# Kernel tuning notes

Measured on AMD Instinct MI355X. Metric: run time of the kernel, lower is better.

## Reference

```python
import jax, jax.numpy as jnp
import numpy as np

B, N, C = 4, 2048, 1024
H = 8
D = C // H  # head dim = 128
SCALE = D ** -0.5
EPS = 1e-5


def setup_inputs() -> dict:
    key = jax.random.key(0)
    ks = jax.random.split(key, 12)
    s = 0.02
    return {
        "x": jax.random.normal(ks[0], (B, N, C), jnp.float32),
        "ln1_g": jnp.ones((C,), jnp.float32),
        "ln1_b": jnp.zeros((C,), jnp.float32),
        "w_qkv": jax.random.normal(ks[1], (3 * C, C), jnp.float32) * s,  # torch Linear weight [out,in], no bias
        "w_proj": jax.random.normal(ks[2], (C, C), jnp.float32) * s,
        "b_proj": jnp.zeros((C,), jnp.float32),
        "ln2_g": jnp.ones((C,), jnp.float32),
        "ln2_b": jnp.zeros((C,), jnp.float32),
        "w1": jax.random.normal(ks[3], (C, C), jnp.float32) * s,
        "b1": jnp.full((C,), 0.1, jnp.float32),
        "w2": jax.random.normal(ks[4], (C, C), jnp.float32) * s,
        "b2": jnp.full((C,), 0.1, jnp.float32),
        "bn_g": jnp.ones((C,), jnp.float32),
        "bn_b": jnp.zeros((C,), jnp.float32),
        "bn_mean": jnp.zeros((C,), jnp.float32),
        "bn_var": jnp.ones((C,), jnp.float32),
    }


def _layernorm(x, g, b):
    mu = jnp.mean(x, axis=-1, keepdims=True)
    var = jnp.mean(jnp.square(x - mu), axis=-1, keepdims=True)
    return (x - mu) * jax.lax.rsqrt(var + EPS) * g + b


def reference(x, ln1_g, ln1_b, w_qkv, w_proj, b_proj, ln2_g, ln2_b,
              w1, b1, w2, b2, bn_g, bn_b, bn_mean, bn_var):
    # --- attention branch (pre-LN) ---
    h = _layernorm(x, ln1_g, ln1_b)
    qkv = h @ w_qkv.T                              # [B,N,3C]
    qkv = qkv.reshape(B, N, 3, H, D)
    q = qkv[:, :, 0].transpose(0, 2, 1, 3)         # [B,H,N,D]
    k = qkv[:, :, 1].transpose(0, 2, 1, 3)
    v = qkv[:, :, 2].transpose(0, 2, 1, 3)
    attn = jnp.einsum('bhnd,bhmd->bhnm', q, k) * SCALE
    attn = jax.nn.softmax(attn, axis=-1)
    o = jnp.einsum('bhnm,bhmd->bhnd', attn, v)     # [B,H,N,D]
    o = o.transpose(0, 2, 1, 3).reshape(B, N, C)
    x = x + (o @ w_proj.T + b_proj)

    # --- MLP branch (pre-LN), ELU + eval-mode BatchNorm ---
    h = _layernorm(x, ln2_g, ln2_b)
    h = jax.nn.elu(h @ w1.T + b1)
    h = jax.nn.elu(h @ w2.T + b2)
    h = (h - bn_mean) * jax.lax.rsqrt(bn_var + EPS) * bn_g + bn_b
    return x + h
```

## Files before the change

kernel.cpp:

```cpp
#include <hip/hip_runtime.h>
#include <hip/hip_bf16.h>

using u16 = unsigned short;
typedef __attribute__((ext_vector_type(8))) __bf16 bf16x8;
typedef __attribute__((ext_vector_type(4))) float f32x4;
typedef __attribute__((ext_vector_type(16))) float f32x16;
typedef __attribute__((ext_vector_type(4))) unsigned int u32x4;
typedef __attribute__((ext_vector_type(2))) unsigned int u32x2;

#define LN_EPS 1e-5f
#define ATT_SCALE 0.08838834764831845f

__device__ __forceinline__ u16 f2bf(float f) {
    unsigned int u = __builtin_bit_cast(unsigned int, f);
    u += 0x7FFFu + ((u >> 16) & 1u);
    return (u16)(u >> 16);
}

__device__ __forceinline__ bf16x8 ld_frag(const u16* p) {
    return __builtin_bit_cast(bf16x8, *(const u32x4*)p);
}

__device__ __forceinline__ unsigned pack_bf2(float lo, float hi) {
    return __builtin_amdgcn_perm(__builtin_bit_cast(unsigned, hi),
                                 __builtin_bit_cast(unsigned, lo), 0x07060302u);
}

__device__ __forceinline__ void gl_lds(const u16* g, u16* l) {
    __builtin_amdgcn_global_load_lds((const __attribute__((address_space(1))) void*)g,
                                     (__attribute__((address_space(3))) void*)l, 16, 0, 0);
}

__global__ __launch_bounds__(256)
void cvt_ln(const float* __restrict__ x, const float* __restrict__ g,
            const float* __restrict__ b, u16* __restrict__ hout,
            const float* __restrict__ w_qkv, const float* __restrict__ w_proj,
            const float* __restrict__ w1, const float* __restrict__ w2,
            u16* __restrict__ wout)
{
    const int t = threadIdx.x;
    if (blockIdx.x < 8192) {
        const int row = blockIdx.x;
        const float4 v = ((const float4*)(x + (size_t)row * 1024))[t];
        float s  = v.x + v.y + v.z + v.w;
        float ss = v.x * v.x + v.y * v.y + v.z * v.z + v.w * v.w;
        #pragma unroll
        for (int d = 32; d > 0; d >>= 1) { s += __shfl_down(s, d); ss += __shfl_down(ss, d); }
        __shared__ float red[8];
        const int wave = t >> 6, lane = t & 63;
        if (lane == 0) { red[wave] = s; red[4 + wave] = ss; }
        __syncthreads();
        const float S  = red[0] + red[1] + red[2] + red[3];
        const float SS = red[4] + red[5] + red[6] + red[7];
        const float mu = S * (1.f / 1024.f);
        const float rstd = rsqrtf(SS * (1.f / 1024.f) - mu * mu + LN_EPS);
        const float4 gv = ((const float4*)g)[t];
        const float4 bv = ((const float4*)b)[t];
        ushort4 ov;
        ov.x = f2bf((v.x - mu) * rstd * gv.x + bv.x);
        ov.y = f2bf((v.y - mu) * rstd * gv.y + bv.y);
        ov.z = f2bf((v.z - mu) * rstd * gv.z + bv.z);
        ov.w = f2bf((v.w - mu) * rstd * gv.w + bv.w);
        ((ushort4*)(hout + (size_t)row * 1024))[t] = ov;
    } else {
        const int i = (blockIdx.x - 8192) * 256 + t;
        const int n_qkv = 3072 * 1024 / 4, n_c = 1024 * 1024 / 4;
        const float* src;
        int j = i;
        if (j < n_qkv) { src = w_qkv; }
        else if ((j -= n_qkv) < n_c) { src = w_proj; }
        else if ((j -= n_c) < n_c)   { src = w1; }
        else { j -= n_c; src = w2; }
        const float4 v = ((const float4*)src)[j];
        ushort4 o;
        o.x = f2bf(v.x); o.y = f2bf(v.y); o.z = f2bf(v.z); o.w = f2bf(v.w);
        ((ushort4*)wout)[i] = o;
    }
}

__global__ __launch_bounds__(256)
void ln_kernel(const float* __restrict__ x, const float* __restrict__ g,
               const float* __restrict__ b, u16* __restrict__ out)
{
    const int row = blockIdx.x;
    const int t = threadIdx.x;
    const float4 v = ((const float4*)(x + (size_t)row * 1024))[t];
    float s  = v.x + v.y + v.z + v.w;
    float ss = v.x * v.x + v.y * v.y + v.z * v.z + v.w * v.w;
    #pragma unroll
    for (int d = 32; d > 0; d >>= 1) { s += __shfl_down(s, d); ss += __shfl_down(ss, d); }
    __shared__ float red[8];
    const int wave = t >> 6, lane = t & 63;
    if (lane == 0) { red[wave] = s; red[4 + wave] = ss; }
    __syncthreads();
    const float S  = red[0] + red[1] + red[2] + red[3];
    const float SS = red[4] + red[5] + red[6] + red[7];
    const float mu = S * (1.f / 1024.f);
    const float rstd = rsqrtf(SS * (1.f / 1024.f) - mu * mu + LN_EPS);
    const float4 gv = ((const float4*)g)[t];
    const float4 bv = ((const float4*)b)[t];
    ushort4 ov;
    ov.x = f2bf((v.x - mu) * rstd * gv.x + bv.x);
    ov.y = f2bf((v.y - mu) * rstd * gv.y + bv.y);
    ov.z = f2bf((v.z - mu) * rstd * gv.z + bv.z);
    ov.w = f2bf((v.w - mu) * rstd * gv.w + bv.w);
    ((ushort4*)(out + (size_t)row * 1024))[t] = ov;
}


#define GEMM_PREAMBLE(Aptr, Bptr, Kdim)                                           \
    __shared__ __align__(16) u16 As[128 * 64];                                    \
    __shared__ __align__(16) u16 Bs[128 * 64];                                    \
    const int tid  = threadIdx.x;                                                 \
    const int wave = tid >> 6;                                                    \
    const int lane = tid & 63;                                                    \
    const int quad = lane >> 4;                                                   \
    const int l16  = lane & 15;                                                   \
    const int m0 = blockIdx.x * 128;                                              \
    const int n0 = blockIdx.y * 128;                                              \
    const int wm = (wave & 1) * 64;                                               \
    const int wn = (wave >> 1) * 64;                                              \
    f32x4 acc[4][4];                                                              \
    _Pragma("unroll")                                                             \
    for (int i = 0; i < 4; i++)                                                   \
        _Pragma("unroll")                                                         \
        for (int j = 0; j < 4; j++)                                               \
            acc[i][j] = f32x4{0.f, 0.f, 0.f, 0.f};                                \
    const int srow8 = lane >> 3;                  \
    const int scol  = ((lane & 7) ^ srow8) * 8;    \
    const u16* gA = Aptr + (size_t)(m0 + wave * 8 + srow8) * Kdim + scol;         \
    const u16* gB = Bptr + (size_t)(n0 + wave * 8 + srow8) * Kdim + scol;         \
    u16* lA = &As[wave * 512];                                                    \
    u16* lB = &Bs[wave * 512];                                                    \
    for (int k0 = 0; k0 < Kdim; k0 += 64) {                                       \
        _Pragma("unroll")                                                         \
        for (int rnd = 0; rnd < 4; rnd++) {                                       \
            gl_lds(gA + (size_t)rnd * 32 * Kdim + k0, lA + rnd * 2048);           \
            gl_lds(gB + (size_t)rnd * 32 * Kdim + k0, lB + rnd * 2048);           \
        }                                                                         \
        __syncthreads();                                                          \
        _Pragma("unroll")                                                         \
        for (int kk = 0; kk < 2; kk++) {                                          \
            bf16x8 af[4], bfv[4];                                                 \
            _Pragma("unroll")                                                     \
            for (int i = 0; i < 4; i++) {                                         \
                const int row = wm + i * 16 + l16;                                \
                const int c = (kk * 4 + quad) ^ (row & 7);                        \
                af[i] = ld_frag(&As[row * 64 + c * 8]);                           \
            }                                                                     \
            _Pragma("unroll")                                                     \
            for (int j = 0; j < 4; j++) {                                         \
                const int row = wn + j * 16 + l16;                                \
                const int c = (kk * 4 + quad) ^ (row & 7);                        \
                bfv[j] = ld_frag(&Bs[row * 64 + c * 8]);                          \
            }                                                                     \
            _Pragma("unroll")                                                     \
            for (int i = 0; i < 4; i++)                                           \
                _Pragma("unroll")                                                 \
                for (int j = 0; j < 4; j++)                                       \
                    acc[i][j] = __builtin_amdgcn_mfma_f32_16x16x32_bf16(          \
                        af[i], bfv[j], acc[i][j], 0, 0, 0);                       \
        }                                                                         \
        __syncthreads();                                                          \
    }

__global__ __launch_bounds__(256, 3)
void gemm_qkv(const u16* __restrict__ A, const u16* __restrict__ Bw,
              u16* __restrict__ Cb, u16* __restrict__ Cv)
{
    GEMM_PREAMBLE(A, Bw, 1024)

    #pragma unroll
    for (int j = 0; j < 4; j++) {
        const int gn = n0 + wn + j * 16 + l16;
        if (gn < 2048) {
            const float qs = (gn < 1024) ? ATT_SCALE : 1.0f;
            #pragma unroll
            for (int i = 0; i < 4; i++) {
                const int gm0 = m0 + wm + i * 16 + quad * 4;
                #pragma unroll
                for (int r = 0; r < 4; r++)
                    Cb[(size_t)(gm0 + r) * 2048 + gn] = f2bf(acc[i][j][r] * qs);
            }
        } else {
            const int hh = (gn >> 7) & 7, dd = gn & 127;
            #pragma unroll
            for (int i = 0; i < 4; i++) {
                const int gm0 = m0 + wm + i * 16 + quad * 4;
                #pragma unroll
                for (int r = 0; r < 4; r++) {
                    const int tok = gm0 + r;
                    Cv[((size_t)((tok >> 11) * 8 + hh) * 128 + dd) * 2048 + (tok & 2047)] =
                        f2bf(acc[i][j][r]);
                }
            }
        }
    }
}

template <int EPI>
__global__ __launch_bounds__(256, 3)
void gemm_c(const u16* __restrict__ A, const u16* __restrict__ Bw,
            const float* __restrict__ bias, const float* __restrict__ res,
            float* __restrict__ Cf, u16* __restrict__ Cb,
            const float* __restrict__ bng, const float* __restrict__ bnb,
            const float* __restrict__ bnm, const float* __restrict__ bnv)
{
    const int N = 1024;
    GEMM_PREAMBLE(A, Bw, 1024)

    #pragma unroll
    for (int j = 0; j < 4; j++) {
        const int gn = n0 + wn + j * 16 + l16;
        float bs = bias[gn], sc = 0.f, sh = 0.f;
        if constexpr (EPI == 3) {
            const float iv = rsqrtf(bnv[gn] + LN_EPS);
            sc = bng[gn] * iv;
            sh = bnb[gn] - bnm[gn] * sc;
        }
        #pragma unroll
        for (int i = 0; i < 4; i++) {
            const int gm0 = m0 + wm + i * 16 + quad * 4;
            #pragma unroll
            for (int r = 0; r < 4; r++) {
                const size_t idx = (size_t)(gm0 + r) * N + gn;
                const float v = acc[i][j][r];
                if constexpr (EPI == 1) {
                    Cf[idx] = res[idx] + v + bs;
                } else if constexpr (EPI == 2) {
                    float t = v + bs;
                    t = t > 0.f ? t : (__expf(t) - 1.f);
                    Cb[idx] = f2bf(t);
                } else {
                    float t = v + bs;
                    t = t > 0.f ? t : (__expf(t) - 1.f);
                    t = t * sc + sh;
                    Cf[idx] = res[idx] + t;
                }
            }
        }
    }
}

__global__ __launch_bounds__(256, 2)
void attn_kernel(const u16* __restrict__ qk, const u16* __restrict__ vT, u16* __restrict__ o)
{
    __shared__ __align__(16) u16 smem[32768];

    const int tid  = threadIdx.x;
    const int wave = tid >> 6;
    const int lane = tid & 63;
    const int l32  = lane & 31;
    const int hl   = lane >> 5;
    const int id   = blockIdx.x;
    const int bh   = ((id >> 7) << 3) | (id & 7);
    const int qt   = (id >> 3) & 15;
    const int b    = bh >> 3, h = bh & 7;
    const size_t tok0 = (size_t)b * 2048;

    const u16* qptr = qk + h * 128;
    const u16* kptr = qk + 1024 + h * 128;
    const u16* vptr = vT + (size_t)bh * 128 * 2048;

    #pragma unroll
    for (int qq = 0; qq < 8; qq++) {
        const int s = qq * 256 + tid;
        const int r = s >> 4;
        const int cg = (s & 15) ^ (r & 7);
        const u16* g = qptr + (tok0 + qt * 128 + r) * 2048 + cg * 8;
        const int sb = 16384 + (qq * 256 + (tid & 192)) * 8;
        gl_lds(g, smem + sb);
    }
    __syncthreads();

    bf16x8 qf[8];
    {
        const int row = wave * 32 + l32;
        #pragma unroll
        for (int ks = 0; ks < 8; ks++) {
            const int c = (ks * 2 + hl) ^ (row & 7);
            qf[ks] = ld_frag(smem + 16384 + row * 128 + c * 8);
        }
    }

    f32x16 oacc[4];
    #pragma unroll
    for (int i = 0; i < 4; i++)
        #pragma unroll
        for (int e = 0; e < 16; e++) oacc[i][e] = 0.f;
    float l_acc = 0.f;

    {
        #pragma unroll
        for (int qq = 0; qq < 4; qq++) {
            const int s = qq * 256 + tid;
            const int rk = s >> 4, ck = (s & 15) ^ (rk & 7);
            gl_lds(kptr + (tok0 + rk) * 2048 + ck * 8,
                   smem + (qq * 256 + (tid & 192)) * 8);
            const int rv = s >> 3, cv = (s & 7) ^ (rv & 7);
            gl_lds(vptr + (size_t)rv * 2048 + cv * 8,
                   smem + 8192 + (qq * 256 + (tid & 192)) * 8);
        }
    }

    for (int kt = 0; kt < 32; kt++) {
        __syncthreads();

        if (kt + 1 < 32) {
            u16* nb = smem + ((kt + 1) & 1) * 16384;
            #pragma unroll
            for (int qq = 0; qq < 4; qq++) {
                const int s = qq * 256 + tid;
                const int rk = s >> 4, ck = (s & 15) ^ (rk & 7);
                gl_lds(kptr + (tok0 + (kt + 1) * 64 + rk) * 2048 + ck * 8,
                       nb + (qq * 256 + (tid & 192)) * 8);
                const int rv = s >> 3, cv = (s & 7) ^ (rv & 7);
                gl_lds(vptr + (size_t)rv * 2048 + (kt + 1) * 64 + cv * 8,
                       nb + 8192 + (qq * 256 + (tid & 192)) * 8);
            }
        }

        const u16* Ks = smem + (kt & 1) * 16384;
        const u16* Vs = Ks + 8192;

        f32x16 sacc[2];
        #pragma unroll
        for (int t = 0; t < 2; t++)
            #pragma unroll
            for (int e = 0; e < 16; e++) sacc[t][e] = 0.f;
        __builtin_amdgcn_s_setprio(1);
        #pragma unroll
        for (int ks = 0; ks < 8; ks++) {
            #pragma unroll
            for (int mt = 0; mt < 2; mt++) {
                const int row = mt * 32 + l32;
                const int c = (ks * 2 + hl) ^ (row & 7);
                const bf16x8 kf = ld_frag(Ks + row * 128 + c * 8);
                sacc[mt] = __builtin_amdgcn_mfma_f32_32x32x16_bf16(kf, qf[ks], sacc[mt], 0, 0, 0);
            }
        }
        __builtin_amdgcn_s_setprio(0);

        unsigned pk[2][8];
        #pragma unroll
        for (int t = 0; t < 2; t++) {
            #pragma unroll
            for (int r2 = 0; r2 < 8; r2++) {
                const float p0 = __expf(sacc[t][2 * r2]);
                const float p1 = __expf(sacc[t][2 * r2 + 1]);
                l_acc += p0 + p1;
                pk[t][r2] = pack_bf2(p0, p1);
            }
        }

        #pragma unroll
        for (int ks = 0; ks < 4; ks++) {
            const int t = ks >> 1;
            const int pb = (ks & 1) * 4;
            const u32x2 r02 = __builtin_amdgcn_permlane32_swap(pk[t][pb + 0], pk[t][pb + 2], false, false);
            const u32x2 r13 = __builtin_amdgcn_permlane32_swap(pk[t][pb + 1], pk[t][pb + 3], false, false);
            u32x4 pu;
            pu.x = r02.x; pu.y = r13.x; pu.z = r02.y; pu.w = r13.y;
            const bf16x8 pf = __builtin_bit_cast(bf16x8, pu);
            __builtin_amdgcn_s_setprio(1);
            #pragma unroll
            for (int dt = 0; dt < 4; dt++) {
                const int row = dt * 32 + l32;
                const int c = (ks * 2 + hl) ^ (row & 7);
                const bf16x8 vf = ld_frag(Vs + row * 64 + c * 8);
                oacc[dt] = __builtin_amdgcn_mfma_f32_32x32x16_bf16(vf, pf, oacc[dt], 0, 0, 0);
            }
            __builtin_amdgcn_s_setprio(0);
        }
    }

    __syncthreads();
    u16* Ot = smem;
    const float lt  = l_acc + __shfl_xor(l_acc, 32);
    const float inv = 1.0f / lt;
    const int qloc = wave * 32 + l32;
    #pragma unroll
    for (int dt = 0; dt < 4; dt++) {
        #pragma unroll
        for (int r2 = 0; r2 < 8; r2++) {
            const float v0 = oacc[dt][2 * r2] * inv;
            const float v1 = oacc[dt][2 * r2 + 1] * inv;
            const int dp = dt * 32 + 4 * hl + 2 * (r2 & 1) + 8 * (r2 >> 1);
            *(unsigned*)(Ot + qloc * 136 + dp) = pack_bf2(v0, v1);
        }
    }
    __syncthreads();
    const int qr = tid >> 1;
    const int hh = tid & 1;
    const u16* src = Ot + qr * 136 + hh * 64;
    u16* dst = o + (tok0 + qt * 128 + qr) * 1024 + h * 128 + hh * 64;
    #pragma unroll
    for (int c = 0; c < 8; c++)
        *(u32x4*)(dst + c * 8) = *(const u32x4*)(src + c * 8);
}

extern "C" void kernel_launch(void* const* d_in, const int* in_sizes, int n_in,
                              void* d_out, int out_size, void* d_ws, size_t ws_size,
                              hipStream_t stream)
{
    const float* x      = (const float*)d_in[0];
    const float* ln1_g  = (const float*)d_in[1];
    const float* ln1_b  = (const float*)d_in[2];
    const float* w_qkv  = (const float*)d_in[3];
    const float* w_proj = (const float*)d_in[4];
    const float* b_proj = (const float*)d_in[5];
    const float* ln2_g  = (const float*)d_in[6];
    const float* ln2_b  = (const float*)d_in[7];
    const float* w1     = (const float*)d_in[8];
    const float* b1     = (const float*)d_in[9];
    const float* w2     = (const float*)d_in[10];
    const float* b2     = (const float*)d_in[11];
    const float* bn_g   = (const float*)d_in[12];
    const float* bn_b   = (const float*)d_in[13];
    const float* bn_m   = (const float*)d_in[14];
    const float* bn_v   = (const float*)d_in[15];
    float* out = (float*)d_out;

    u16* wq   = (u16*)d_ws;
    u16* wp   = wq  + (size_t)3072 * 1024;
    u16* w1b  = wp  + (size_t)1024 * 1024;
    u16* w2b  = w1b + (size_t)1024 * 1024;
    u16* hbuf = w2b + (size_t)1024 * 1024;
    u16* qkb  = hbuf + (size_t)8192 * 1024;
    u16* vTb  = qkb + (size_t)8192 * 2048;
    u16* obuf = vTb + (size_t)8192 * 1024;
    float* x1 = (float*)(obuf + (size_t)8192 * 1024);

    cvt_ln<<<14336, 256, 0, stream>>>(x, ln1_g, ln1_b, hbuf, w_qkv, w_proj, w1, w2, wq);

    gemm_qkv<<<dim3(64, 24), 256, 0, stream>>>(hbuf, wq, qkb, vTb);

    attn_kernel<<<512, 256, 0, stream>>>(qkb, vTb, obuf);

    gemm_c<1><<<dim3(64, 8), 256, 0, stream>>>(obuf, wp,
        b_proj, x, x1, nullptr, nullptr, nullptr, nullptr, nullptr);

    ln_kernel<<<8192, 256, 0, stream>>>(x1, ln2_g, ln2_b, hbuf);

    gemm_c<2><<<dim3(64, 8), 256, 0, stream>>>(hbuf, w1b,
        b1, nullptr, nullptr, obuf, nullptr, nullptr, nullptr, nullptr);

    gemm_c<3><<<dim3(64, 8), 256, 0, stream>>>(obuf, w2b,
        b2, x1, out, nullptr, bn_g, bn_b, bn_m, bn_v);
}
```

Before: 361.8 us.

## Process two query sub-tiles per wave in attention to reuse K/V fragments

The attention kernel now handles 256 queries per block, 64 per wave, as two 32-row sub-tiles, instead of 128. Each K and V fragment loaded from LDS feeds two MFMAs, which halves LDS traffic and the K/V global loads per query. The grid shrinks to 256 blocks with launch bounds relaxed to one block per SM, and the output writeback is split into two phases through shared memory. In exchange, register pressure roughly doubles for the accumulators, occupancy drops, and 256 blocks may not fill all compute units well.

```diff
diff --git a/kernel.cpp b/kernel.cpp
--- a/kernel.cpp
+++ b/kernel.cpp
@@ -107,7 +107,6 @@
     ((ushort4*)(out + (size_t)row * 1024))[t] = ov;
 }
 
-
 #define GEMM_PREAMBLE(Aptr, Bptr, Kdim)                                           \
     __shared__ __align__(16) u16 As[128 * 64];                                    \
     __shared__ __align__(16) u16 Bs[128 * 64];                                    \
@@ -126,8 +125,8 @@
         _Pragma("unroll")                                                         \
         for (int j = 0; j < 4; j++)                                               \
             acc[i][j] = f32x4{0.f, 0.f, 0.f, 0.f};                                \
-    const int srow8 = lane >> 3;                  \
-    const int scol  = ((lane & 7) ^ srow8) * 8;    \
+    const int srow8 = lane >> 3;                                                  \
+    const int scol  = ((lane & 7) ^ srow8) * 8;                                   \
     const u16* gA = Aptr + (size_t)(m0 + wave * 8 + srow8) * Kdim + scol;         \
     const u16* gB = Bptr + (size_t)(n0 + wave * 8 + srow8) * Kdim + scol;         \
     u16* lA = &As[wave * 512];                                                    \
@@ -242,7 +241,7 @@
     }
 }
 
-__global__ __launch_bounds__(256, 2)
+__global__ __launch_bounds__(256, 1)
 void attn_kernel(const u16* __restrict__ qk, const u16* __restrict__ vT, u16* __restrict__ o)
 {
     __shared__ __align__(16) u16 smem[32768];
@@ -253,8 +252,8 @@
     const int l32  = lane & 31;
     const int hl   = lane >> 5;
     const int id   = blockIdx.x;
-    const int bh   = ((id >> 7) << 3) | (id & 7);
-    const int qt   = (id >> 3) & 15;
+    const int bh   = id & 31;
+    const int qt   = id >> 5;
     const int b    = bh >> 3, h = bh & 7;
     const size_t tok0 = (size_t)b * 2048;
 
@@ -263,32 +262,35 @@
     const u16* vptr = vT + (size_t)bh * 128 * 2048;
 
     #pragma unroll
-    for (int qq = 0; qq < 8; qq++) {
+    for (int qq = 0; qq < 16; qq++) {
         const int s = qq * 256 + tid;
         const int r = s >> 4;
         const int cg = (s & 15) ^ (r & 7);
-        const u16* g = qptr + (tok0 + qt * 128 + r) * 2048 + cg * 8;
-        const int sb = 16384 + (qq * 256 + (tid & 192)) * 8;
-        gl_lds(g, smem + sb);
+        gl_lds(qptr + (tok0 + qt * 256 + r) * 2048 + cg * 8,
+               smem + (qq * 256 + (tid & 192)) * 8);
     }
     __syncthreads();
 
-    bf16x8 qf[8];
-    {
-        const int row = wave * 32 + l32;
+    bf16x8 qf[2][8];
+    #pragma unroll
+    for (int qh = 0; qh < 2; qh++) {
+        const int row = wave * 64 + qh * 32 + l32;
         #pragma unroll
         for (int ks = 0; ks < 8; ks++) {
             const int c = (ks * 2 + hl) ^ (row & 7);
-            qf[ks] = ld_frag(smem + 16384 + row * 128 + c * 8);
-        }
-    }
-
-    f32x16 oacc[4];
+            qf[qh][ks] = ld_frag(smem + row * 128 + c * 8);
+        }
+    }
+    __syncthreads();
+
+    f32x16 oacc[4][2];
     #pragma unroll
     for (int i = 0; i < 4; i++)
         #pragma unroll
-        for (int e = 0; e < 16; e++) oacc[i][e] = 0.f;
-    float l_acc = 0.f;
+        for (int qh = 0; qh < 2; qh++)
+            #pragma unroll
+            for (int e = 0; e < 16; e++) oacc[i][qh][e] = 0.f;
+    float l_acc[2] = {0.f, 0.f};
 
     {
         #pragma unroll
@@ -323,11 +325,13 @@
         const u16* Ks = smem + (kt & 1) * 16384;
         const u16* Vs = Ks + 8192;
 
-        f32x16 sacc[2];
+        f32x16 sacc[2][2];
         #pragma unroll
         for (int t = 0; t < 2; t++)
             #pragma unroll
-            for (int e = 0; e < 16; e++) sacc[t][e] = 0.f;
+            for (int qh = 0; qh < 2; qh++)
+                #pragma unroll
+                for (int e = 0; e < 16; e++) sacc[t][qh][e] = 0.f;
         __builtin_amdgcn_s_setprio(1);
         #pragma unroll
         for (int ks = 0; ks < 8; ks++) {
@@ -336,20 +340,26 @@
                 const int row = mt * 32 + l32;
                 const int c = (ks * 2 + hl) ^ (row & 7);
                 const bf16x8 kf = ld_frag(Ks + row * 128 + c * 8);
-                sacc[mt] = __builtin_amdgcn_mfma_f32_32x32x16_bf16(kf, qf[ks], sacc[mt], 0, 0, 0);
+                #pragma unroll
+                for (int qh = 0; qh < 2; qh++)
+                    sacc[mt][qh] = __builtin_amdgcn_mfma_f32_32x32x16_bf16(
+                        kf, qf[qh][ks], sacc[mt][qh], 0, 0, 0);
             }
         }
         __builtin_amdgcn_s_setprio(0);
 
-        unsigned pk[2][8];
+        unsigned pk[2][2][8];
         #pragma unroll
         for (int t = 0; t < 2; t++) {
             #pragma unroll
-            for (int r2 = 0; r2 < 8; r2++) {
-                const float p0 = __expf(sacc[t][2 * r2]);
-                const float p1 = __expf(sacc[t][2 * r2 + 1]);
-                l_acc += p0 + p1;
-                pk[t][r2] = pack_bf2(p0, p1);
+            for (int qh = 0; qh < 2; qh++) {
+                #pragma unroll
+                for (int r2 = 0; r2 < 8; r2++) {
+                    const float p0 = __expf(sacc[t][qh][2 * r2]);
+                    const float p1 = __expf(sacc[t][qh][2 * r2 + 1]);
+                    l_acc[qh] += p0 + p1;
+                    pk[t][qh][r2] = pack_bf2(p0, p1);
+                }
             }
         }
 
@@ -357,46 +367,64 @@
         for (int ks = 0; ks < 4; ks++) {
             const int t = ks >> 1;
             const int pb = (ks & 1) * 4;
-            const u32x2 r02 = __builtin_amdgcn_permlane32_swap(pk[t][pb + 0], pk[t][pb + 2], false, false);
-            const u32x2 r13 = __builtin_amdgcn_permlane32_swap(pk[t][pb + 1], pk[t][pb + 3], false, false);
-            u32x4 pu;
-            pu.x = r02.x; pu.y = r13.x; pu.z = r02.y; pu.w = r13.y;
-            const bf16x8 pf = __builtin_bit_cast(bf16x8, pu);
-            __builtin_amdgcn_s_setprio(1);
+            bf16x8 vf[4];
             #pragma unroll
             for (int dt = 0; dt < 4; dt++) {
                 const int row = dt * 32 + l32;
                 const int c = (ks * 2 + hl) ^ (row & 7);
-                const bf16x8 vf = ld_frag(Vs + row * 64 + c * 8);
-                oacc[dt] = __builtin_amdgcn_mfma_f32_32x32x16_bf16(vf, pf, oacc[dt], 0, 0, 0);
-            }
-            __builtin_amdgcn_s_setprio(0);
-        }
-    }
-
-    __syncthreads();
-    u16* Ot = smem;
-    const float lt  = l_acc + __shfl_xor(l_acc, 32);
-    const float inv = 1.0f / lt;
-    const int qloc = wave * 32 + l32;
-    #pragma unroll
-    for (int dt = 0; dt < 4; dt++) {
-        #pragma unroll
-        for (int r2 = 0; r2 < 8; r2++) {
-            const float v0 = oacc[dt][2 * r2] * inv;
-            const float v1 = oacc[dt][2 * r2 + 1] * inv;
-            const int dp = dt * 32 + 4 * hl + 2 * (r2 & 1) + 8 * (r2 >> 1);
-            *(unsigned*)(Ot + qloc * 136 + dp) = pack_bf2(v0, v1);
-        }
-    }
-    __syncthreads();
-    const int qr = tid >> 1;
-    const int hh = tid & 1;
-    const u16* src = Ot + qr * 136 + hh * 64;
-    u16* dst = o + (tok0 + qt * 128 + qr) * 1024 + h * 128 + hh * 64;
-    #pragma unroll
-    for (int c = 0; c < 8; c++)
-        *(u32x4*)(dst + c * 8) = *(const u32x4*)(src + c * 8);
+                vf[dt] = ld_frag(Vs + row * 64 + c * 8);
+            }
+            #pragma unroll
+            for (int qh = 0; qh < 2; qh++) {
+                const u32x2 r02 = __builtin_amdgcn_permlane32_swap(pk[t][qh][pb + 0], pk[t][qh][pb + 2], false, false);
+                const u32x2 r13 = __builtin_amdgcn_permlane32_swap(pk[t][qh][pb + 1], pk[t][qh][pb + 3], false, false);
+                u32x4 pu;
+                pu.x = r02.x; pu.y = r13.x; pu.z = r02.y; pu.w = r13.y;
+                const bf16x8 pf = __builtin_bit_cast(bf16x8, pu);
+                __builtin_amdgcn_s_setprio(1);
+                #pragma unroll
+                for (int dt = 0; dt < 4; dt++)
+                    oacc[dt][qh] = __builtin_amdgcn_mfma_f32_32x32x16_bf16(
+                        vf[dt], pf, oacc[dt][qh], 0, 0, 0);
+                __builtin_amdgcn_s_setprio(0);
+            }
+        }
+    }
+
+    const float lt0 = l_acc[0] + __shfl_xor(l_acc[0], 32);
+    const float lt1 = l_acc[1] + __shfl_xor(l_acc[1], 32);
+    const float inv0 = 1.0f / lt0;
+    const float inv1 = 1.0f / lt1;
+
+    #pragma unroll
+    for (int ph = 0; ph < 2; ph++) {
+        __syncthreads();
+        if ((wave >> 1) == ph) {
+            #pragma unroll
+            for (int qh = 0; qh < 2; qh++) {
+                const float inv = (qh == 0) ? inv0 : inv1;
+                const int qloc = (wave & 1) * 64 + qh * 32 + l32;
+                #pragma unroll
+                for (int dt = 0; dt < 4; dt++) {
+                    #pragma unroll
+                    for (int r2 = 0; r2 < 8; r2++) {
+                        const float v0 = oacc[dt][qh][2 * r2] * inv;
+                        const float v1 = oacc[dt][qh][2 * r2 + 1] * inv;
+                        const int dp = dt * 32 + 4 * hl + 2 * (r2 & 1) + 8 * (r2 >> 1);
+                        *(unsigned*)(smem + qloc * 136 + dp) = pack_bf2(v0, v1);
+                    }
+                }
+            }
+        }
+        __syncthreads();
+        const int qr = tid >> 1;
+        const int hh = tid & 1;
+        const u16* src = smem + qr * 136 + hh * 64;
+        u16* dst = o + (tok0 + qt * 256 + ph * 128 + qr) * 1024 + h * 128 + hh * 64;
+        #pragma unroll
+        for (int c = 0; c < 8; c++)
+            *(u32x4*)(dst + c * 8) = *(const u32x4*)(src + c * 8);
+    }
 }
 
 extern "C" void kernel_launch(void* const* d_in, const int* in_sizes, int n_in,
@@ -435,7 +463,7 @@
 
     gemm_qkv<<<dim3(64, 24), 256, 0, stream>>>(hbuf, wq, qkb, vTb);
 
-    attn_kernel<<<512, 256, 0, stream>>>(qkb, vTb, obuf);
+    attn_kernel<<<256, 256, 0, stream>>>(qkb, vTb, obuf);
 
     gemm_c<1><<<dim3(64, 8), 256, 0, stream>>>(obuf, wp,
         b_proj, x, x1, nullptr, nullptr, nullptr, nullptr, nullptr);
```

After: 392.1 us. 1.08x slower.

## Split attention KV tile across wave pairs, each wave owning 64 query rows

Applied to the files above, without the earlier changes.

Each wave now handles 64 query rows (two 32-row subtiles) but only half of each 64-key tile. Every K and V fragment loaded from LDS therefore feeds two MFMAs, which halves LDS reads per MFMA. The two key-halves' partial outputs and row sums are merged through shared memory at the end. The cost is double the accumulator registers (128 fp32 for oacc), which puts the 2-blocks-per-CU occupancy at risk, plus an extra reduction stage with two more barriers.

```diff
diff --git a/kernel.cpp b/kernel.cpp
--- a/kernel.cpp
+++ b/kernel.cpp
@@ -107,7 +107,6 @@
     ((ushort4*)(out + (size_t)row * 1024))[t] = ov;
 }
 
-
 #define GEMM_PREAMBLE(Aptr, Bptr, Kdim)                                           \
     __shared__ __align__(16) u16 As[128 * 64];                                    \
     __shared__ __align__(16) u16 Bs[128 * 64];                                    \
@@ -126,8 +125,8 @@
         _Pragma("unroll")                                                         \
         for (int j = 0; j < 4; j++)                                               \
             acc[i][j] = f32x4{0.f, 0.f, 0.f, 0.f};                                \
-    const int srow8 = lane >> 3;                  \
-    const int scol  = ((lane & 7) ^ srow8) * 8;    \
+    const int srow8 = lane >> 3;                                                  \
+    const int scol  = ((lane & 7) ^ srow8) * 8;                                   \
     const u16* gA = Aptr + (size_t)(m0 + wave * 8 + srow8) * Kdim + scol;         \
     const u16* gB = Bptr + (size_t)(n0 + wave * 8 + srow8) * Kdim + scol;         \
     u16* lA = &As[wave * 512];                                                    \
@@ -245,13 +244,15 @@
 __global__ __launch_bounds__(256, 2)
 void attn_kernel(const u16* __restrict__ qk, const u16* __restrict__ vT, u16* __restrict__ o)
 {
-    __shared__ __align__(16) u16 smem[32768];
+    __shared__ __align__(16) u16 smem[33024];
 
     const int tid  = threadIdx.x;
     const int wave = tid >> 6;
     const int lane = tid & 63;
     const int l32  = lane & 31;
     const int hl   = lane >> 5;
+    const int qh2  = wave & 1;
+    const int kh   = wave >> 1;
     const int id   = blockIdx.x;
     const int bh   = ((id >> 7) << 3) | (id & 7);
     const int qt   = (id >> 3) & 15;
@@ -273,22 +274,25 @@
     }
     __syncthreads();
 
-    bf16x8 qf[8];
-    {
-        const int row = wave * 32 + l32;
+    bf16x8 qf[2][8];
+    #pragma unroll
+    for (int qs = 0; qs < 2; qs++) {
+        const int row = qh2 * 64 + qs * 32 + l32;
         #pragma unroll
         for (int ks = 0; ks < 8; ks++) {
             const int c = (ks * 2 + hl) ^ (row & 7);
-            qf[ks] = ld_frag(smem + 16384 + row * 128 + c * 8);
-        }
-    }
-
-    f32x16 oacc[4];
+            qf[qs][ks] = ld_frag(smem + 16384 + row * 128 + c * 8);
+        }
+    }
+
+    f32x16 oacc[4][2];
     #pragma unroll
     for (int i = 0; i < 4; i++)
         #pragma unroll
-        for (int e = 0; e < 16; e++) oacc[i][e] = 0.f;
-    float l_acc = 0.f;
+        for (int qs = 0; qs < 2; qs++)
+            #pragma unroll
+            for (int e = 0; e < 16; e++) oacc[i][qs][e] = 0.f;
+    float l_acc[2] = {0.f, 0.f};
 
     {
         #pragma unroll
@@ -325,68 +329,125 @@
 
         f32x16 sacc[2];
         #pragma unroll
-        for (int t = 0; t < 2; t++)
-            #pragma unroll
-            for (int e = 0; e < 16; e++) sacc[t][e] = 0.f;
+        for (int qs = 0; qs < 2; qs++)
+            #pragma unroll
+            for (int e = 0; e < 16; e++) sacc[qs][e] = 0.f;
         __builtin_amdgcn_s_setprio(1);
         #pragma unroll
         for (int ks = 0; ks < 8; ks++) {
-            #pragma unroll
-            for (int mt = 0; mt < 2; mt++) {
-                const int row = mt * 32 + l32;
-                const int c = (ks * 2 + hl) ^ (row & 7);
-                const bf16x8 kf = ld_frag(Ks + row * 128 + c * 8);
-                sacc[mt] = __builtin_amdgcn_mfma_f32_32x32x16_bf16(kf, qf[ks], sacc[mt], 0, 0, 0);
-            }
+            const int row = kh * 32 + l32;
+            const int c = (ks * 2 + hl) ^ (row & 7);
+            const bf16x8 kf = ld_frag(Ks + row * 128 + c * 8);
+            #pragma unroll
+            for (int qs = 0; qs < 2; qs++)
+                sacc[qs] = __builtin_amdgcn_mfma_f32_32x32x16_bf16(kf, qf[qs][ks], sacc[qs], 0, 0, 0);
         }
         __builtin_amdgcn_s_setprio(0);
 
         unsigned pk[2][8];
         #pragma unroll
-        for (int t = 0; t < 2; t++) {
+        for (int qs = 0; qs < 2; qs++) {
             #pragma unroll
             for (int r2 = 0; r2 < 8; r2++) {
-                const float p0 = __expf(sacc[t][2 * r2]);
-                const float p1 = __expf(sacc[t][2 * r2 + 1]);
-                l_acc += p0 + p1;
-                pk[t][r2] = pack_bf2(p0, p1);
-            }
-        }
-
-        #pragma unroll
-        for (int ks = 0; ks < 4; ks++) {
-            const int t = ks >> 1;
-            const int pb = (ks & 1) * 4;
-            const u32x2 r02 = __builtin_amdgcn_permlane32_swap(pk[t][pb + 0], pk[t][pb + 2], false, false);
-            const u32x2 r13 = __builtin_amdgcn_permlane32_swap(pk[t][pb + 1], pk[t][pb + 3], false, false);
-            u32x4 pu;
-            pu.x = r02.x; pu.y = r13.x; pu.z = r02.y; pu.w = r13.y;
-            const bf16x8 pf = __builtin_bit_cast(bf16x8, pu);
-            __builtin_amdgcn_s_setprio(1);
+                const float p0 = __expf(sacc[qs][2 * r2]);
+                const float p1 = __expf(sacc[qs][2 * r2 + 1]);
+                l_acc[qs] += p0 + p1;
+                pk[qs][r2] = pack_bf2(p0, p1);
+            }
+        }
+
+        #pragma unroll
+        for (int ks2 = 0; ks2 < 2; ks2++) {
+            bf16x8 vf[4];
             #pragma unroll
             for (int dt = 0; dt < 4; dt++) {
                 const int row = dt * 32 + l32;
-                const int c = (ks * 2 + hl) ^ (row & 7);
-                const bf16x8 vf = ld_frag(Vs + row * 64 + c * 8);
-                oacc[dt] = __builtin_amdgcn_mfma_f32_32x32x16_bf16(vf, pf, oacc[dt], 0, 0, 0);
-            }
-            __builtin_amdgcn_s_setprio(0);
+                const int c = (kh * 4 + ks2 * 2 + hl) ^ (row & 7);
+                vf[dt] = ld_frag(Vs + row * 64 + c * 8);
+            }
+            #pragma unroll
+            for (int qs = 0; qs < 2; qs++) {
+                const int pb = ks2 * 4;
+                const u32x2 r02 = __builtin_amdgcn_permlane32_swap(pk[qs][pb + 0], pk[qs][pb + 2], false, false);
+                const u32x2 r13 = __builtin_amdgcn_permlane32_swap(pk[qs][pb + 1], pk[qs][pb + 3], false, false);
+                u32x4 pu;
+                pu.x = r02.x; pu.y = r13.x; pu.z = r02.y; pu.w = r13.y;
+                const bf16x8 pf = __builtin_bit_cast(bf16x8, pu);
+                __builtin_amdgcn_s_setprio(1);
+                #pragma unroll
+                for (int dt = 0; dt < 4; dt++)
+                    oacc[dt][qs] = __builtin_amdgcn_mfma_f32_32x32x16_bf16(vf[dt], pf, oacc[dt][qs], 0, 0, 0);
+                __builtin_amdgcn_s_setprio(0);
+            }
         }
     }
 
     __syncthreads();
+    float lt[2];
+    lt[0] = l_acc[0] + __shfl_xor(l_acc[0], 32);
+    lt[1] = l_acc[1] + __shfl_xor(l_acc[1], 32);
+
+    float* const ox = (float*)smem;
+    float* const lx = (float*)(smem + 32768);
+
+    if (kh == 1) {
+        #pragma unroll
+        for (int qs = 0; qs < 2; qs++) {
+            #pragma unroll
+            for (int dt = 0; dt < 4; dt++) {
+                const int base16 = qh2 * 2048 + qs * 1024 + dt * 256;
+                #pragma unroll
+                for (int c = 0; c < 4; c++) {
+                    const int cc = c ^ (lane & 3);
+                    const int ch = base16 + lane * 4 + cc;
+                    *(f32x4*)(ox + ch * 4) = f32x4{oacc[dt][qs][cc * 4 + 0],
+                                                   oacc[dt][qs][cc * 4 + 1],
+                                                   oacc[dt][qs][cc * 4 + 2],
+                                                   oacc[dt][qs][cc * 4 + 3]};
+                }
+            }
+            if (hl == 0) lx[qh2 * 64 + qs * 32 + l32] = lt[qs];
+        }
+    }
+    __syncthreads();
+    if (kh == 0) {
+        #pragma unroll
+        for (int qs = 0; qs < 2; qs++) {
+            #pragma unroll
+            for (int dt = 0; dt < 4; dt++) {
+                const int base16 = qh2 * 2048 + qs * 1024 + dt * 256;
+                #pragma unroll
+                for (int c = 0; c < 4; c++) {
+                    const int cc = c ^ (lane & 3);
+                    const int ch = base16 + lane * 4 + cc;
+                    const f32x4 v = *(const f32x4*)(ox + ch * 4);
+                    oacc[dt][qs][cc * 4 + 0] += v[0];
+                    oacc[dt][qs][cc * 4 + 1] += v[1];
+                    oacc[dt][qs][cc * 4 + 2] += v[2];
+                    oacc[dt][qs][cc * 4 + 3] += v[3];
+                }
+            }
+            lt[qs] += lx[qh2 * 64 + qs * 32 + l32];
+        }
+    }
+    __syncthreads();
+
     u16* Ot = smem;
-    const float lt  = l_acc + __shfl_xor(l_acc, 32);
-    const float inv = 1.0f / lt;
-    const int qloc = wave * 32 + l32;
-    #pragma unroll
-    for (int dt = 0; dt < 4; dt++) {
-        #pragma unroll
-        for (int r2 = 0; r2 < 8; r2++) {
-            const float v0 = oacc[dt][2 * r2] * inv;
-            const float v1 = oacc[dt][2 * r2 + 1] * inv;
-            const int dp = dt * 32 + 4 * hl + 2 * (r2 & 1) + 8 * (r2 >> 1);
-            *(unsigned*)(Ot + qloc * 136 + dp) = pack_bf2(v0, v1);
+    if (kh == 0) {
+        #pragma unroll
+        for (int qs = 0; qs < 2; qs++) {
+            const float inv = 1.0f / lt[qs];
+            const int qloc = qh2 * 64 + qs * 32 + l32;
+            #pragma unroll
+            for (int dt = 0; dt < 4; dt++) {
+                #pragma unroll
+                for (int r2 = 0; r2 < 8; r2++) {
+                    const float v0 = oacc[dt][qs][2 * r2] * inv;
+                    const float v1 = oacc[dt][qs][2 * r2 + 1] * inv;
+                    const int dp = dt * 32 + 4 * hl + 2 * (r2 & 1) + 8 * (r2 >> 1);
+                    *(unsigned*)(Ot + qloc * 136 + dp) = pack_bf2(v0, v1);
+                }
+            }
         }
     }
     __syncthreads();
```

New measurement: 529.0 us. 46.2% more time.

## Double-buffer GEMM LDS tiles to overlap global loads with MFMA

Applied to the files above, without the earlier changes.

Converts the shared GEMM main loop to a two-stage LDS ping-pong. The next K tile is prefetched with direct global-to-LDS loads while MFMAs run on the current tile, and one barrier per iteration replaces two. It also raises wave priority around the MFMA block and lowers the launch-bounds occupancy hint from 3 to 2 to account for the doubled LDS use. The cost is lower occupancy and a possible hazard, since gl_lds writes must be complete before the next barrier's reads.

```diff
diff --git a/kernel.cpp b/kernel.cpp
--- a/kernel.cpp
+++ b/kernel.cpp
@@ -107,10 +107,9 @@
     ((ushort4*)(out + (size_t)row * 1024))[t] = ov;
 }
 
-
 #define GEMM_PREAMBLE(Aptr, Bptr, Kdim)                                           \
-    __shared__ __align__(16) u16 As[128 * 64];                                    \
-    __shared__ __align__(16) u16 Bs[128 * 64];                                    \
+    __shared__ __align__(16) u16 As[2][128 * 64];                                 \
+    __shared__ __align__(16) u16 Bs[2][128 * 64];                                 \
     const int tid  = threadIdx.x;                                                 \
     const int wave = tid >> 6;                                                    \
     const int lane = tid & 63;                                                    \
@@ -126,19 +125,29 @@
         _Pragma("unroll")                                                         \
         for (int j = 0; j < 4; j++)                                               \
             acc[i][j] = f32x4{0.f, 0.f, 0.f, 0.f};                                \
-    const int srow8 = lane >> 3;                  \
-    const int scol  = ((lane & 7) ^ srow8) * 8;    \
+    const int srow8 = lane >> 3;                                                  \
+    const int scol  = ((lane & 7) ^ srow8) * 8;                                   \
     const u16* gA = Aptr + (size_t)(m0 + wave * 8 + srow8) * Kdim + scol;         \
     const u16* gB = Bptr + (size_t)(n0 + wave * 8 + srow8) * Kdim + scol;         \
-    u16* lA = &As[wave * 512];                                                    \
-    u16* lB = &Bs[wave * 512];                                                    \
-    for (int k0 = 0; k0 < Kdim; k0 += 64) {                                       \
-        _Pragma("unroll")                                                         \
-        for (int rnd = 0; rnd < 4; rnd++) {                                       \
-            gl_lds(gA + (size_t)rnd * 32 * Kdim + k0, lA + rnd * 2048);           \
-            gl_lds(gB + (size_t)rnd * 32 * Kdim + k0, lB + rnd * 2048);           \
+    _Pragma("unroll")                                                             \
+    for (int rnd = 0; rnd < 4; rnd++) {                                           \
+        gl_lds(gA + (size_t)rnd * 32 * Kdim, &As[0][wave * 512 + rnd * 2048]);    \
+        gl_lds(gB + (size_t)rnd * 32 * Kdim, &Bs[0][wave * 512 + rnd * 2048]);    \
+    }                                                                             \
+    const int NT = Kdim / 64;                                                     \
+    for (int t = 0; t < NT; t++) {                                                \
+        __syncthreads();  \
+        if (t + 1 < NT) {                                                         \
+            u16* dA = &As[(t + 1) & 1][wave * 512];                               \
+            u16* dB = &Bs[(t + 1) & 1][wave * 512];                               \
+            _Pragma("unroll")                                                     \
+            for (int rnd = 0; rnd < 4; rnd++) {                                   \
+                gl_lds(gA + (size_t)rnd * 32 * Kdim + (t + 1) * 64, dA + rnd * 2048); \
+                gl_lds(gB + (size_t)rnd * 32 * Kdim + (t + 1) * 64, dB + rnd * 2048); \
+            }                                                                     \
         }                                                                         \
-        __syncthreads();                                                          \
+        const u16* curA = As[t & 1];                                              \
+        const u16* curB = Bs[t & 1];                                              \
         _Pragma("unroll")                                                         \
         for (int kk = 0; kk < 2; kk++) {                                          \
             bf16x8 af[4], bfv[4];                                                 \
@@ -146,25 +155,26 @@
             for (int i = 0; i < 4; i++) {                                         \
                 const int row = wm + i * 16 + l16;                                \
                 const int c = (kk * 4 + quad) ^ (row & 7);                        \
-                af[i] = ld_frag(&As[row * 64 + c * 8]);                           \
+                af[i] = ld_frag(&curA[row * 64 + c * 8]);                         \
             }                                                                     \
             _Pragma("unroll")                                                     \
             for (int j = 0; j < 4; j++) {                                         \
                 const int row = wn + j * 16 + l16;                                \
                 const int c = (kk * 4 + quad) ^ (row & 7);                        \
-                bfv[j] = ld_frag(&Bs[row * 64 + c * 8]);                          \
+                bfv[j] = ld_frag(&curB[row * 64 + c * 8]);                        \
             }                                                                     \
+            __builtin_amdgcn_s_setprio(1);                                        \
             _Pragma("unroll")                                                     \
             for (int i = 0; i < 4; i++)                                           \
                 _Pragma("unroll")                                                 \
                 for (int j = 0; j < 4; j++)                                       \
                     acc[i][j] = __builtin_amdgcn_mfma_f32_16x16x32_bf16(          \
                         af[i], bfv[j], acc[i][j], 0, 0, 0);                       \
+            __builtin_amdgcn_s_setprio(0);                                        \
         }                                                                         \
-        __syncthreads();                                                          \
-    }
-
-__global__ __launch_bounds__(256, 3)
+    }
+
+__global__ __launch_bounds__(256, 2)
 void gemm_qkv(const u16* __restrict__ A, const u16* __restrict__ Bw,
               u16* __restrict__ Cb, u16* __restrict__ Cv)
 {
@@ -199,7 +209,7 @@
 }
 
 template <int EPI>
-__global__ __launch_bounds__(256, 3)
+__global__ __launch_bounds__(256, 2)
 void gemm_c(const u16* __restrict__ A, const u16* __restrict__ Bw,
             const float* __restrict__ bias, const float* __restrict__ res,
             float* __restrict__ Cf, u16* __restrict__ Cb,
```

New measurement: 353.0 us (median of 4 runs). 2.4% less time.
